# Kernel tuning notes

Measured on AMD Instinct MI355X. Metric: run time of the kernel, lower is better.

The kernel has to match this reference:

```python
import jax, jax.numpy as jnp
import numpy as np

B, T, I, H, O = 128, 256, 64, 512, 1
G = 4 * H


def setup_inputs() -> dict:
    key = jax.random.key(0)
    ks = jax.random.split(key, 16)
    s = 1.0 / np.sqrt(H)  # PyTorch LSTM/Linear init scale

    def u(k, shape):
        return jax.random.uniform(k, shape, jnp.float32, -s, s)

    return {
        "x": jax.random.normal(ks[0], (B, T, I), jnp.float32),
        "w_ih_0f": u(ks[1], (G, I)), "w_hh_0f": u(ks[2], (G, H)), "b_0f": u(ks[3], (G,)),
        "w_ih_0b": u(ks[4], (G, I)), "w_hh_0b": u(ks[5], (G, H)), "b_0b": u(ks[6], (G,)),
        "w_ih_1f": u(ks[7], (G, 2 * H)), "w_hh_1f": u(ks[8], (G, H)), "b_1f": u(ks[9], (G,)),
        "w_ih_1b": u(ks[10], (G, 2 * H)), "w_hh_1b": u(ks[11], (G, H)), "b_1b": u(ks[12], (G,)),
        "fc_w": u(ks[13], (O, 2 * H)), "fc_b": u(ks[14], (O,)),
    }


def _lstm_dir(x, w_ih, w_hh, b, reverse):
    # x: [B, T, F]. Precompute input projection for all timesteps (one big GEMM).
    xp = jnp.einsum('btf,gf->btg', x, w_ih) + b  # [B, T, 4H]

    def step(carry, xt):
        h, c = carry
        gates = xt + h @ w_hh.T  # [B, 4H]
        i, f, g, o = jnp.split(gates, 4, axis=-1)  # PyTorch gate order i,f,g,o
        c = jax.nn.sigmoid(f) * c + jax.nn.sigmoid(i) * jnp.tanh(g)
        h = jax.nn.sigmoid(o) * jnp.tanh(c)
        return (h, c), h

    h0 = jnp.zeros((x.shape[0], H), x.dtype)
    (_, _), hs = jax.lax.scan(step, (h0, h0), jnp.swapaxes(xp, 0, 1), reverse=reverse)
    return jnp.swapaxes(hs, 0, 1)  # [B, T, H], time-aligned with input


def reference(x, w_ih_0f, w_hh_0f, b_0f, w_ih_0b, w_hh_0b, b_0b,
              w_ih_1f, w_hh_1f, b_1f, w_ih_1b, w_hh_1b, b_1b, fc_w, fc_b):
    h = jnp.concatenate([_lstm_dir(x, w_ih_0f, w_hh_0f, b_0f, False),
                         _lstm_dir(x, w_ih_0b, w_hh_0b, b_0b, True)], axis=-1)
    h = jnp.concatenate([_lstm_dir(h, w_ih_1f, w_hh_1f, b_1f, False),
                         _lstm_dir(h, w_ih_1b, w_hh_1b, b_1b, True)], axis=-1)
    return h[:, -1, :] @ fc_w.T + fc_b  # [B, O]
```

## Files before the change

kernel.cpp:

```cpp
#include <hip/hip_runtime.h>

#define HB 65536
#define NBLK 256

typedef unsigned short u16;
typedef unsigned long long u64;
typedef __attribute__((ext_vector_type(8))) short bf16x8;
typedef __attribute__((ext_vector_type(8))) _Float16 f16x8;
typedef __attribute__((ext_vector_type(4))) float f32x4;
typedef __attribute__((ext_vector_type(2))) unsigned long long u64x2;
typedef __attribute__((ext_vector_type(8))) short s16x8;

#define MFMA_F16(a, b, c) __builtin_amdgcn_mfma_f32_16x16x32_f16(a, b, c, 0, 0, 0)
#define MFMA_BF16(a, b, c) __builtin_amdgcn_mfma_f32_16x16x32_bf16(a, b, c, 0, 0, 0)

__device__ __forceinline__ float fsig(float x) { return 1.f / (1.f + __expf(-x)); }
__device__ __forceinline__ float ftanh(float x) {
  float e = __expf(2.f * x);
  return 1.f - 2.f / (e + 1.f);
}
__device__ __forceinline__ u16 f2bf(float f) {
  unsigned u = __builtin_bit_cast(unsigned, f);
  return (u16)((u + 0x7FFFu + ((u >> 16) & 1)) >> 16);
}
__device__ __forceinline__ float bf2f(u16 h) {
  unsigned u = ((unsigned)h) << 16;
  return __builtin_bit_cast(float, u);
}
__device__ __forceinline__ u16 f2h(float f) {
  _Float16 h = (_Float16)f;
  return __builtin_bit_cast(u16, h);
}

__device__ __forceinline__ u64 at_ld64(const void* p) {
  return __hip_atomic_load((const u64*)p, __ATOMIC_RELAXED, __HIP_MEMORY_SCOPE_AGENT);
}
__device__ __forceinline__ void at_st64(void* p, u64 v) {
  __hip_atomic_store((u64*)p, v, __ATOMIC_RELAXED, __HIP_MEMORY_SCOPE_AGENT);
}
__device__ __forceinline__ unsigned at_ld32(const void* p) {
  return __hip_atomic_load((const unsigned*)p, __ATOMIC_RELAXED, __HIP_MEMORY_SCOPE_AGENT);
}
__device__ __forceinline__ void at_st32(void* p, unsigned v) {
  __hip_atomic_store((unsigned*)p, v, __ATOMIC_RELAXED, __HIP_MEMORY_SCOPE_AGENT);
}
__device__ __forceinline__ u64 pk4(u16 a, u16 b, u16 c, u16 d) {
  return (u64)a | ((u64)b << 16) | ((u64)c << 32) | ((u64)d << 48);
}
__device__ __forceinline__ u64 pkf2(float a, float b) {
  return (u64)__builtin_bit_cast(unsigned, a) | ((u64)__builtin_bit_cast(unsigned, b) << 32);
}

template <bool F16>
__global__ void pack_w(const float* __restrict__ W, u16* __restrict__ dst, int K) {
  int NKT = K >> 5;
  long gid = (long)blockIdx.x * 256 + threadIdx.x;
  long total = (long)128 * NKT * 64;
  if (gid >= total) return;
  int lane = gid & 63;
  int kt = (gid >> 6) % NKT;
  int rt = (gid >> 6) / NKT;
  int r = lane & 15;
  int grow = (r >> 2) * 512 + rt * 4 + (r & 3);
  int k0 = kt * 32 + (lane >> 4) * 8;
  long base = ((long)(rt * NKT + kt) * 2) * 512 + lane * 8;
#pragma unroll
  for (int e = 0; e < 8; ++e) {
    float w = W[(long)grow * K + k0 + e];
    u16 hi, lo;
    if (F16) {
      _Float16 h = (_Float16)w;
      hi = __builtin_bit_cast(u16, h);
      _Float16 l2 = (_Float16)(w - (float)h);
      lo = __builtin_bit_cast(u16, l2);
    } else {
      hi = f2bf(w);
      lo = f2bf(w - bf2f(hi));
    }
    dst[base + e] = hi;
    dst[base + 512 + e] = lo;
  }
}

__global__ void pack_x(const float* __restrict__ x, u16* __restrict__ xp) {
  long gid = (long)blockIdx.x * 256 + threadIdx.x;
  if (gid >= 128L * 256 * 64) return;
  int k = gid & 63;
  long bt = gid >> 6;
  int t = bt & 255;
  int b = bt >> 8;
  xp[((long)t * 128 + b) * 64 + k] = f2h(x[((long)b * 256 + t) * 64 + k]);
}

__global__ void pack_bias(const float* __restrict__ b0f, const float* __restrict__ b0b,
                          const float* __restrict__ b1f, const float* __restrict__ b1b,
                          float* __restrict__ bp) {
  int gid = blockIdx.x * 256 + threadIdx.x;
  if (gid >= 8192) return;
  int src = gid >> 11;
  int idx = gid & 2047;
  int rt = idx >> 4, rr = idx & 15;
  int grow = (rr >> 2) * 512 + rt * 4 + (rr & 3);
  const float* B = (src == 0) ? b0f : (src == 1) ? b0b : (src == 2) ? b1f : b1b;
  bp[gid] = B[grow];
}

#define C_TRANS 0
#define C_FIN 64

__global__ __launch_bounds__(512, 2) void lstm_persist(
    const u16* __restrict__ xpack, u16* __restrict__ h0arch,
    const u16* __restrict__ wih0f_p, const u16* __restrict__ wih0b_p,
    const u16* __restrict__ whh0f_p, const u16* __restrict__ whh0b_p,
    const u16* __restrict__ wih1f_p, const u16* __restrict__ whh1f_p,
    const u16* __restrict__ wih1b_p, const u16* __restrict__ whh1b_p,
    const float* __restrict__ biasP,
    u16* __restrict__ hl0, u16* __restrict__ hl1,
    float* __restrict__ h1bf32,
    const float* __restrict__ fcw, const float* __restrict__ fcb,
    float* __restrict__ out,
    unsigned* __restrict__ flagsA, unsigned* __restrict__ flagsB,
    unsigned* __restrict__ cnt) {
  const int bid = blockIdx.x;
  const int xcd = bid & 7, slot = bid >> 3;
  const int tid = threadIdx.x;
  const int wid = tid >> 6, l = tid & 63;
  const int c = l & 15, q = l >> 4;

  __shared__ __align__(16) char smem[65536];
  __shared__ __align__(16) f32x4 shacc[8][2][64];

  const f32x4 fz = {0.f, 0.f, 0.f, 0.f};

  auto arriveflag = [&](unsigned* fl, unsigned gen) {
    asm volatile("s_waitcnt vmcnt(0)" ::: "memory");
    __syncthreads();
    if (tid == 0) at_st32(fl + (long)bid * 64, gen);
  };
  auto waitflags = [&](const unsigned* fl, int base, int nmem, unsigned gen) {
    if (wid == 0) {
      unsigned f;
      do {
        f = (l < nmem) ? at_ld32(fl + (long)(base + l) * 64) : gen;
      } while (__ballot(f < gen));
    }
    __syncthreads();
  };
  auto arrivecnt = [&](int idx) {
    asm volatile("s_waitcnt vmcnt(0)" ::: "memory");
    __syncthreads();
    if (tid == 0)
      __hip_atomic_fetch_add(cnt + idx, 1u, __ATOMIC_RELAXED, __HIP_MEMORY_SCOPE_AGENT);
  };
  auto waitcnt_ = [&](int idx, unsigned tgt) {
    if (tid == 0) {
      while (at_ld32(cnt + idx) < tgt) __builtin_amdgcn_s_sleep(1);
    }
    __syncthreads();
  };

  {
    const int d = slot >> 4;
    const int bg = (slot >> 2) & 3;
    const int gbase = d * 128 + bg * 32;
    const int ug = xcd * 4 + (slot & 3);
    const int rowt = ug * 4 + (wid >> 1);
    const int kh = wid & 1;
    const u16* wxp = d ? wih0b_p : wih0f_p;
    const u16* whp = d ? whh0b_p : whh0f_p;
    const int b0e = bg * 32 + kh * 16;
    const float* bp = biasP + ((long)d * 128 + rowt) * 16 + q * 4;

    f16x8 wxh, wxl;
    {
      const u16* a = wxp + ((long)(rowt * 2 + kh) * 2) * 512 + l * 8;
      wxh = *(const f16x8*)a;
      wxl = *(const f16x8*)(a + 512);
    }
    bf16x8 whh_r[8], whl_r[8];
#pragma unroll
    for (int j = 0; j < 8; ++j) {
      const u16* a = whp + ((long)(rowt * 16 + kh * 8 + j) * 2) * 512 + l * 8;
      whh_r[j] = *(const bf16x8*)a;
      whl_r[j] = *(const bf16x8*)(a + 512);
    }

    const int sw = (c & 7) << 4;
    const int cq0 = (c << 10) | (q << 4);
    const int cq1 = ((16 + c) << 10) | (q << 4);

    float c_reg[4] = {0.f, 0.f, 0.f, 0.f};
    for (int s = 0; s < 256; ++s) {
      const int t = d ? 255 - s : s;
      const int par = s & 1;
      f32x4 acc0 = fz, acc1 = fz;
      {
        const u16* xb = xpack + ((long)t * 128 + bg * 32 + c) * 64 + kh * 32 + q * 8;
        f16x8 bx0 = *(const f16x8*)xb;
        f16x8 bx1 = *(const f16x8*)(xb + 16 * 64);
        acc0 = MFMA_F16(wxh, bx0, acc0);
        acc0 = MFMA_F16(wxl, bx0, acc0);
        acc1 = MFMA_F16(wxh, bx1, acc1);
        acc1 = MFMA_F16(wxl, bx1, acc1);
      }
      if (s) {
        waitflags(flagsA, gbase, 32, s);
        const u16* hp_hi = hl0 + ((long)(par * 2 + d) * 2) * HB;
        const u16* hp_lo = hp_hi + HB;
#pragma unroll
        for (int i = 0; i < 8; ++i) {
          int m = tid + (i << 9);
          int pl = m >> 11, r = m & 2047;
          int b = r >> 6, k16 = r & 63;
          const u16* src = (pl ? hp_lo : hp_hi) + (long)(bg * 32 + b) * 512 + k16 * 8;
          u64x2 v;
          v.x = at_ld64(src);
          v.y = at_ld64(src + 4);
          int dst = pl * 32768 + (((b << 10) | (k16 << 4)) ^ ((b & 7) << 4));
          *(u64x2*)(smem + dst) = v;
        }
        __syncthreads();
#pragma unroll
        for (int j = 0; j < 8; ++j) {
          const int kt = kh * 8 + j;
          const int b0a = (cq0 | (kt << 6)) ^ sw;
          const int b1a = (cq1 | (kt << 6)) ^ sw;
          bf16x8 bhi0 = *(const bf16x8*)(smem + b0a);
          bf16x8 blo0 = *(const bf16x8*)(smem + 32768 + b0a);
          bf16x8 bhi1 = *(const bf16x8*)(smem + b1a);
          bf16x8 blo1 = *(const bf16x8*)(smem + 32768 + b1a);
          acc0 = MFMA_BF16(whh_r[j], bhi0, acc0);
          acc0 = MFMA_BF16(whl_r[j], bhi0, acc0);
          acc0 = MFMA_BF16(whh_r[j], blo0, acc0);
          acc1 = MFMA_BF16(whh_r[j], bhi1, acc1);
          acc1 = MFMA_BF16(whl_r[j], bhi1, acc1);
          acc1 = MFMA_BF16(whh_r[j], blo1, acc1);
        }
      }
      shacc[wid][0][l] = acc0;
      shacc[wid][1][l] = acc1;
      __syncthreads();
      {
        const int pr = (wid >> 1) * 2;
        const int bo = wid & 1;
        f32x4 tot = shacc[pr][bo][l] + shacc[pr + 1][bo][l];
        float pre[4];
#pragma unroll
        for (int i = 0; i < 4; ++i) pre[i] = tot[i] + bp[i];
        const int par_w = par ^ 1;
        u16* hn_hi = hl0 + ((long)(par_w * 2 + d) * 2) * HB;
        u16* hn_lo = hn_hi + HB;
        const int b = b0e + c;
        u16 pbh[4], pbl[4], pf[4];
#pragma unroll
        for (int i = 0; i < 4; ++i) {
          float gI = __shfl(pre[i], c);
          float gF = __shfl(pre[i], c + 16);
          float gG = __shfl(pre[i], c + 32);
          float gO = __shfl(pre[i], c + 48);
          float cn = fsig(gF) * c_reg[i] + fsig(gI) * ftanh(gG);
          c_reg[i] = cn;
          float hv = fsig(gO) * ftanh(cn);
          u16 hh = f2bf(hv);
          pbh[i] = hh;
          pbl[i] = f2bf(hv - bf2f(hh));
          pf[i] = f2h(hv);
        }
        if (q == 0) {
          if (s < 255) {
            at_st64(hn_hi + (long)b * 512 + rowt * 4, pk4(pbh[0], pbh[1], pbh[2], pbh[3]));
            at_st64(hn_lo + (long)b * 512 + rowt * 4, pk4(pbl[0], pbl[1], pbl[2], pbl[3]));
          }
          at_st64(h0arch + ((long)t * 128 + b) * 1024 + d * 512 + rowt * 4,
                  pk4(pf[0], pf[1], pf[2], pf[3]));
        }
      }
      if (s < 255) arriveflag(flagsA, (unsigned)(s + 1));
      else arrivecnt(C_TRANS);
    }
  }
  waitcnt_(C_TRANS, NBLK);
  __threadfence();
  __syncthreads();

  {
    const int ug1 = xcd * 8 + (slot & 7);
    const int bg1 = slot >> 3;
    const int rl1 = (wid >> 1) & 1;
    const int btl1 = wid & 1;
    const int kh = wid >> 2;
    const int rowt1 = ug1 * 2 + rl1;
    const int b01 = bg1 * 32 + btl1 * 16;
    f32x4 a0 = fz, a1 = fz;
    const u16* bbase = h0arch + (255L * 128 + b01 + c) * 1024 + q * 8;
#pragma unroll
    for (int kk = 0; kk < 16; ++kk) {
      int kt = kh * 16 + kk;
      const u16* a = wih1b_p + ((long)(rowt1 * 32 + kt) * 2) * 512 + l * 8;
      f16x8 ahi = *(const f16x8*)a;
      f16x8 alo = *(const f16x8*)(a + 512);
      f16x8 bx = *(const f16x8*)(bbase + kt * 32);
      f32x4& t0 = (kk & 1) ? a1 : a0;
      t0 = MFMA_F16(ahi, bx, t0);
      t0 = MFMA_F16(alo, bx, t0);
    }
    f32x4 acc = a0 + a1;
    shacc[wid][0][l] = acc;
    __syncthreads();
    if (wid < 4) {
      f32x4 tot = shacc[wid][0][l] + shacc[wid + 4][0][l];
      const float* bp1 = biasP + (3L * 128 + rowt1) * 16 + q * 4;
      float pre[4];
#pragma unroll
      for (int i = 0; i < 4; ++i) pre[i] = tot[i] + bp1[i];
      const int b = b01 + c;
      float hv[4];
#pragma unroll
      for (int i = 0; i < 4; ++i) {
        float gI = __shfl(pre[i], c);
        float gG = __shfl(pre[i], c + 32);
        float gO = __shfl(pre[i], c + 48);
        float cn = fsig(gI) * ftanh(gG);
        hv[i] = fsig(gO) * ftanh(cn);
      }
      if (q == 0) {
        at_st64((u16*)(h1bf32 + (long)b * 512 + rowt1 * 4), pkf2(hv[0], hv[1]));
        at_st64((u16*)(h1bf32 + (long)b * 512 + rowt1 * 4 + 2), pkf2(hv[2], hv[3]));
      }
    }
    __syncthreads();
  }

  {
    const int ug1 = xcd * 8 + (slot & 7);
    const int bg1 = slot >> 3;
    const int g1base = bg1 * 64;
    const int rl1 = wid & 1;
    const int kh1 = wid >> 1;
    const int rowt1 = ug1 * 2 + rl1;

    f16x8 w1h[8], w1l[8];
#pragma unroll
    for (int j = 0; j < 8; ++j) {
      const u16* a = wih1f_p + ((long)(rowt1 * 32 + kh1 * 8 + j) * 2) * 512 + l * 8;
      w1h[j] = *(const f16x8*)a;
      w1l[j] = *(const f16x8*)(a + 512);
    }
    bf16x8 v1h[4], v1l[4];
#pragma unroll
    for (int j = 0; j < 4; ++j) {
      const u16* a = whh1f_p + ((long)(rowt1 * 16 + kh1 * 4 + j) * 2) * 512 + l * 8;
      v1h[j] = *(const bf16x8*)a;
      v1l[j] = *(const bf16x8*)(a + 512);
    }

    const int sw = (c & 7) << 4;
    const int cq0 = (c << 10) | (q << 4);
    const int cq1 = ((16 + c) << 10) | (q << 4);
    const int rl_o = wid & 1;
    const int bt_o = wid >> 1;
    const int rowt_o = ug1 * 2 + rl_o;
    const float* bp1 = biasP + (2L * 128 + rowt_o) * 16 + q * 4;

    float c_reg[4] = {0.f, 0.f, 0.f, 0.f};
    for (int s = 0; s < 256; ++s) {
      const int par = s & 1;
      f32x4 acc0 = fz, acc1 = fz;
      {
        const u16* hb = h0arch + ((long)s * 128 + bg1 * 32 + c) * 1024 + q * 8;
#pragma unroll
        for (int j = 0; j < 8; ++j) {
          const int kt = kh1 * 8 + j;
          f16x8 bx0 = *(const f16x8*)(hb + kt * 32);
          f16x8 bx1 = *(const f16x8*)(hb + 16 * 1024 + kt * 32);
          acc0 = MFMA_F16(w1h[j], bx0, acc0);
          acc0 = MFMA_F16(w1l[j], bx0, acc0);
          acc1 = MFMA_F16(w1h[j], bx1, acc1);
          acc1 = MFMA_F16(w1l[j], bx1, acc1);
        }
      }
      if (s) {
        waitflags(flagsB, g1base, 64, s);
        const u16* hp_hi = hl1 + (long)(par * 2) * HB;
        const u16* hp_lo = hp_hi + HB;
#pragma unroll
        for (int i = 0; i < 8; ++i) {
          int m = tid + (i << 9);
          int pl = m >> 11, r = m & 2047;
          int b = r >> 6, k16 = r & 63;
          const u16* src = (pl ? hp_lo : hp_hi) + (long)(bg1 * 32 + b) * 512 + k16 * 8;
          u64x2 v;
          v.x = at_ld64(src);
          v.y = at_ld64(src + 4);
          int dst = pl * 32768 + (((b << 10) | (k16 << 4)) ^ ((b & 7) << 4));
          *(u64x2*)(smem + dst) = v;
        }
        __syncthreads();
#pragma unroll
        for (int j = 0; j < 4; ++j) {
          const int kt = kh1 * 4 + j;
          const int b0a = (cq0 | (kt << 6)) ^ sw;
          const int b1a = (cq1 | (kt << 6)) ^ sw;
          bf16x8 bhi0 = *(const bf16x8*)(smem + b0a);
          bf16x8 blo0 = *(const bf16x8*)(smem + 32768 + b0a);
          bf16x8 bhi1 = *(const bf16x8*)(smem + b1a);
          bf16x8 blo1 = *(const bf16x8*)(smem + 32768 + b1a);
          acc0 = MFMA_BF16(v1h[j], bhi0, acc0);
          acc0 = MFMA_BF16(v1l[j], bhi0, acc0);
          acc0 = MFMA_BF16(v1h[j], blo0, acc0);
          acc1 = MFMA_BF16(v1h[j], bhi1, acc1);
          acc1 = MFMA_BF16(v1l[j], bhi1, acc1);
          acc1 = MFMA_BF16(v1h[j], blo1, acc1);
        }
      }
      shacc[wid][0][l] = acc0;
      shacc[wid][1][l] = acc1;
      __syncthreads();
      if (wid < 4) {
        f32x4 tot = shacc[rl_o][bt_o][l] + shacc[2 + rl_o][bt_o][l] +
                    shacc[4 + rl_o][bt_o][l] + shacc[6 + rl_o][bt_o][l];
        float pre[4];
#pragma unroll
        for (int i = 0; i < 4; ++i) pre[i] = tot[i] + bp1[i];
        const int par_w = par ^ 1;
        u16* hn_hi = hl1 + (long)(par_w * 2) * HB;
        u16* hn_lo = hn_hi + HB;
        const int b = bg1 * 32 + bt_o * 16 + c;
        u16 pbh[4], pbl[4];
#pragma unroll
        for (int i = 0; i < 4; ++i) {
          float gI = __shfl(pre[i], c);
          float gF = __shfl(pre[i], c + 16);
          float gG = __shfl(pre[i], c + 32);
          float gO = __shfl(pre[i], c + 48);
          float cn = fsig(gF) * c_reg[i] + fsig(gI) * ftanh(gG);
          c_reg[i] = cn;
          float hv = fsig(gO) * ftanh(cn);
          u16 hh = f2bf(hv);
          pbh[i] = hh;
          pbl[i] = f2bf(hv - bf2f(hh));
        }
        if (q == 0) {
          if (s < 255) {
            at_st64(hn_hi + (long)b * 512 + rowt_o * 4, pk4(pbh[0], pbh[1], pbh[2], pbh[3]));
            at_st64(hn_lo + (long)b * 512 + rowt_o * 4, pk4(pbl[0], pbl[1], pbl[2], pbl[3]));
          } else {
            at_st64(hl1 + (long)b * 512 + rowt_o * 4, pk4(pbh[0], pbh[1], pbh[2], pbh[3]));
            at_st64(hl1 + HB + (long)b * 512 + rowt_o * 4, pk4(pbl[0], pbl[1], pbl[2], pbl[3]));
          }
        }
      }
      if (s < 255) arriveflag(flagsB, (unsigned)(s + 1));
      else arrivecnt(C_FIN);
    }
  }
  waitcnt_(C_FIN, NBLK);

  if (bid < 128 && wid == 0) {
    const int b = bid;
    const int j0 = l * 8;
    u64x2 vh, vl;
    vh.x = at_ld64(hl1 + (long)b * 512 + j0);
    vh.y = at_ld64(hl1 + (long)b * 512 + j0 + 4);
    vl.x = at_ld64(hl1 + HB + (long)b * 512 + j0);
    vl.y = at_ld64(hl1 + HB + (long)b * 512 + j0 + 4);
    s16x8 hhi = __builtin_bit_cast(s16x8, vh);
    s16x8 hlo = __builtin_bit_cast(s16x8, vl);
    float ssum = 0.f;
#pragma unroll
    for (int e = 0; e < 8; ++e) {
      int j = j0 + e;
      float hf = bf2f((u16)hhi[e]) + bf2f((u16)hlo[e]);
      unsigned hbu = at_ld32(h1bf32 + (long)b * 512 + j);
      ssum += hf * fcw[j] + __builtin_bit_cast(float, hbu) * fcw[512 + j];
    }
#pragma unroll
    for (int off = 32; off; off >>= 1) ssum += __shfl_down(ssum, off);
    if (l == 0) out[b] = ssum + fcb[0];
  }
}

extern "C" void kernel_launch(void* const* d_in, const int* in_sizes, int n_in,
                              void* d_out, int out_size, void* d_ws, size_t ws_size,
                              hipStream_t stream) {
  const float* x     = (const float*)d_in[0];
  const float* wih0f = (const float*)d_in[1];
  const float* whh0f = (const float*)d_in[2];
  const float* b0f   = (const float*)d_in[3];
  const float* wih0b = (const float*)d_in[4];
  const float* whh0b = (const float*)d_in[5];
  const float* b0b   = (const float*)d_in[6];
  const float* wih1f = (const float*)d_in[7];
  const float* whh1f = (const float*)d_in[8];
  const float* b1f   = (const float*)d_in[9];
  const float* wih1b = (const float*)d_in[10];
  const float* whh1b = (const float*)d_in[11];
  const float* b1b   = (const float*)d_in[12];
  const float* fcw   = (const float*)d_in[13];
  const float* fcb   = (const float*)d_in[14];
  float* out = (float*)d_out;

  char* p = (char*)d_ws;
  auto alloc = [&](size_t bytes) {
    char* r = p;
    p += (bytes + 255) & ~(size_t)255;
    return r;
  };
  u16* xpack   = (u16*)alloc(128L * 256 * 64 * 2);
  u16* wih0f_p = (u16*)alloc(128L * 2 * 2 * 512 * 2);
  u16* wih0b_p = (u16*)alloc(128L * 2 * 2 * 512 * 2);
  u16* whh0f_p = (u16*)alloc(128L * 16 * 2 * 512 * 2);
  u16* whh0b_p = (u16*)alloc(128L * 16 * 2 * 512 * 2);
  u16* wih1f_p = (u16*)alloc(128L * 32 * 2 * 512 * 2);
  u16* whh1f_p = (u16*)alloc(128L * 16 * 2 * 512 * 2);
  u16* wih1b_p = (u16*)alloc(128L * 32 * 2 * 512 * 2);
  u16* whh1b_p = (u16*)alloc(128L * 16 * 2 * 512 * 2);
  float* biasP = (float*)alloc(8192 * 4);
  u16* hl0     = (u16*)alloc(2L * 2 * 2 * HB * 2);
  u16* hl1     = (u16*)alloc(2L * 2 * HB * 2);
  float* h1bf32= (float*)alloc((long)HB * 4);
  unsigned* flagsA = (unsigned*)alloc(256L * 64 * 4);
  unsigned* flagsB = (unsigned*)alloc(256L * 64 * 4);
  unsigned* cnt    = (unsigned*)alloc(128 * 4);
  u16* h0arch  = (u16*)alloc(256L * 128 * 1024 * 2);

  pack_w<true><<<64, 256, 0, stream>>>(wih0f, wih0f_p, 64);
  pack_w<true><<<64, 256, 0, stream>>>(wih0b, wih0b_p, 64);
  pack_w<false><<<512, 256, 0, stream>>>(whh0f, whh0f_p, 512);
  pack_w<false><<<512, 256, 0, stream>>>(whh0b, whh0b_p, 512);
  pack_w<true><<<1024, 256, 0, stream>>>(wih1f, wih1f_p, 1024);
  pack_w<true><<<1024, 256, 0, stream>>>(wih1b, wih1b_p, 1024);
  pack_w<false><<<512, 256, 0, stream>>>(whh1f, whh1f_p, 512);
  pack_w<false><<<512, 256, 0, stream>>>(whh1b, whh1b_p, 512);
  pack_x<<<8192, 256, 0, stream>>>(x, xpack);
  pack_bias<<<32, 256, 0, stream>>>(b0f, b0b, b1f, b1b, biasP);

  (void)hipMemsetAsync(flagsA, 0, 256L * 64 * 4, stream);
  (void)hipMemsetAsync(flagsB, 0, 256L * 64 * 4, stream);
  (void)hipMemsetAsync(cnt, 0, 128 * 4, stream);

  lstm_persist<<<NBLK, 512, 0, stream>>>(
      xpack, h0arch,
      wih0f_p, wih0b_p, whh0f_p, whh0b_p,
      wih1f_p, whh1f_p, wih1b_p, whh1b_p,
      biasP, hl0, hl1, h1bf32,
      fcw, fcb, out, flagsA, flagsB, cnt);
}
```

Before: 3.817 ms.

## Interleave hi/lo bf16 hidden planes and use 128-bit coherent loads/stores

Hidden-state hi and lo bf16 halves are interleaved into one plane with 8-element chunks (4 hi, 4 lo), so each producer writes one 16-byte store instead of two 8-byte atomics. Consumers stage the plane into LDS with batched global_load_dwordx4 using sc0 sc1 cache bits, waiting on all loads at once, and split hi/lo into separate LDS regions. This is meant to cut per-step latency on the cross-block hidden-state exchange in the recurrent loop. It relies on inline asm cache-coherence bits instead of atomics for visibility across blocks.

```diff
diff --git a/kernel.cpp b/kernel.cpp
--- a/kernel.cpp
+++ b/kernel.cpp
@@ -1,7 +1,7 @@
 #include <hip/hip_runtime.h>
 
-#define HB 65536
 #define NBLK 256
+#define PLANE 131072
 
 typedef unsigned short u16;
 typedef unsigned long long u64;
@@ -9,7 +9,6 @@
 typedef __attribute__((ext_vector_type(8))) _Float16 f16x8;
 typedef __attribute__((ext_vector_type(4))) float f32x4;
 typedef __attribute__((ext_vector_type(2))) unsigned long long u64x2;
-typedef __attribute__((ext_vector_type(8))) short s16x8;
 
 #define MFMA_F16(a, b, c) __builtin_amdgcn_mfma_f32_16x16x32_f16(a, b, c, 0, 0, 0)
 #define MFMA_BF16(a, b, c) __builtin_amdgcn_mfma_f32_16x16x32_bf16(a, b, c, 0, 0, 0)
@@ -49,6 +48,9 @@
 }
 __device__ __forceinline__ u64 pkf2(float a, float b) {
   return (u64)__builtin_bit_cast(unsigned, a) | ((u64)__builtin_bit_cast(unsigned, b) << 32);
+}
+__device__ __forceinline__ void st128_cp(u16* p, u64x2 v) {
+  asm volatile("global_store_dwordx4 %0, %1, off sc0 sc1" :: "v"(p), "v"(v) : "memory");
 }
 
 template <bool F16>
@@ -158,6 +160,27 @@
     }
     __syncthreads();
   };
+  auto stage16 = [&](const u16* plane, int b0blk) {
+    u64x2 vv[8];
+#pragma unroll
+    for (int i = 0; i < 8; ++i) {
+      int m = tid + (i << 9);
+      int b = m >> 7, cb = m & 127;
+      const u16* src = plane + ((long)(b0blk + b) << 10) + (cb << 3);
+      asm volatile("global_load_dwordx4 %0, %1, off sc0 sc1"
+                   : "=v"(vv[i]) : "v"(src) : "memory");
+    }
+    asm volatile("s_waitcnt vmcnt(0)" ::: "memory");
+    __builtin_amdgcn_sched_barrier(0);
+#pragma unroll
+    for (int i = 0; i < 8; ++i) {
+      int m = tid + (i << 9);
+      int b = m >> 7, cb = m & 127;
+      int ahi = ((b << 10) | (cb << 3)) ^ ((b & 7) << 4);
+      *(u64*)(smem + ahi) = vv[i].x;
+      *(u64*)(smem + 32768 + ahi) = vv[i].y;
+    }
+  };
 
   {
     const int d = slot >> 4;
@@ -205,20 +228,7 @@
       }
       if (s) {
         waitflags(flagsA, gbase, 32, s);
-        const u16* hp_hi = hl0 + ((long)(par * 2 + d) * 2) * HB;
-        const u16* hp_lo = hp_hi + HB;
-#pragma unroll
-        for (int i = 0; i < 8; ++i) {
-          int m = tid + (i << 9);
-          int pl = m >> 11, r = m & 2047;
-          int b = r >> 6, k16 = r & 63;
-          const u16* src = (pl ? hp_lo : hp_hi) + (long)(bg * 32 + b) * 512 + k16 * 8;
-          u64x2 v;
-          v.x = at_ld64(src);
-          v.y = at_ld64(src + 4);
-          int dst = pl * 32768 + (((b << 10) | (k16 << 4)) ^ ((b & 7) << 4));
-          *(u64x2*)(smem + dst) = v;
-        }
+        stage16(hl0 + (long)(par * 2 + d) * PLANE, bg * 32);
         __syncthreads();
 #pragma unroll
         for (int j = 0; j < 8; ++j) {
@@ -248,8 +258,7 @@
 #pragma unroll
         for (int i = 0; i < 4; ++i) pre[i] = tot[i] + bp[i];
         const int par_w = par ^ 1;
-        u16* hn_hi = hl0 + ((long)(par_w * 2 + d) * 2) * HB;
-        u16* hn_lo = hn_hi + HB;
+        u16* hn = hl0 + (long)(par_w * 2 + d) * PLANE;
         const int b = b0e + c;
         u16 pbh[4], pbl[4], pf[4];
 #pragma unroll
@@ -268,8 +277,10 @@
         }
         if (q == 0) {
           if (s < 255) {
-            at_st64(hn_hi + (long)b * 512 + rowt * 4, pk4(pbh[0], pbh[1], pbh[2], pbh[3]));
-            at_st64(hn_lo + (long)b * 512 + rowt * 4, pk4(pbl[0], pbl[1], pbl[2], pbl[3]));
+            u64x2 pv;
+            pv.x = pk4(pbh[0], pbh[1], pbh[2], pbh[3]);
+            pv.y = pk4(pbl[0], pbl[1], pbl[2], pbl[3]);
+            st128_cp(hn + ((long)b << 10) + rowt * 8, pv);
           }
           at_st64(h0arch + ((long)t * 128 + b) * 1024 + d * 512 + rowt * 4,
                   pk4(pf[0], pf[1], pf[2], pf[3]));
@@ -381,20 +392,7 @@
       }
       if (s) {
         waitflags(flagsB, g1base, 64, s);
-        const u16* hp_hi = hl1 + (long)(par * 2) * HB;
-        const u16* hp_lo = hp_hi + HB;
-#pragma unroll
-        for (int i = 0; i < 8; ++i) {
-          int m = tid + (i << 9);
-          int pl = m >> 11, r = m & 2047;
-          int b = r >> 6, k16 = r & 63;
-          const u16* src = (pl ? hp_lo : hp_hi) + (long)(bg1 * 32 + b) * 512 + k16 * 8;
-          u64x2 v;
-          v.x = at_ld64(src);
-          v.y = at_ld64(src + 4);
-          int dst = pl * 32768 + (((b << 10) | (k16 << 4)) ^ ((b & 7) << 4));
-          *(u64x2*)(smem + dst) = v;
-        }
+        stage16(hl1 + (long)par * PLANE, bg1 * 32);
         __syncthreads();
 #pragma unroll
         for (int j = 0; j < 4; ++j) {
@@ -423,8 +421,7 @@
 #pragma unroll
         for (int i = 0; i < 4; ++i) pre[i] = tot[i] + bp1[i];
         const int par_w = par ^ 1;
-        u16* hn_hi = hl1 + (long)(par_w * 2) * HB;
-        u16* hn_lo = hn_hi + HB;
+        u16* hn = hl1 + (long)par_w * PLANE;
         const int b = bg1 * 32 + bt_o * 16 + c;
         u16 pbh[4], pbl[4];
 #pragma unroll
@@ -441,13 +438,10 @@
           pbl[i] = f2bf(hv - bf2f(hh));
         }
         if (q == 0) {
-          if (s < 255) {
-            at_st64(hn_hi + (long)b * 512 + rowt_o * 4, pk4(pbh[0], pbh[1], pbh[2], pbh[3]));
-            at_st64(hn_lo + (long)b * 512 + rowt_o * 4, pk4(pbl[0], pbl[1], pbl[2], pbl[3]));
-          } else {
-            at_st64(hl1 + (long)b * 512 + rowt_o * 4, pk4(pbh[0], pbh[1], pbh[2], pbh[3]));
-            at_st64(hl1 + HB + (long)b * 512 + rowt_o * 4, pk4(pbl[0], pbl[1], pbl[2], pbl[3]));
-          }
+          u64x2 pv;
+          pv.x = pk4(pbh[0], pbh[1], pbh[2], pbh[3]);
+          pv.y = pk4(pbl[0], pbl[1], pbl[2], pbl[3]);
+          st128_cp(hn + ((long)b << 10) + rowt_o * 8, pv);
         }
       }
       if (s < 255) arriveflag(flagsB, (unsigned)(s + 1));
@@ -458,19 +452,19 @@
 
   if (bid < 128 && wid == 0) {
     const int b = bid;
-    const int j0 = l * 8;
-    u64x2 vh, vl;
-    vh.x = at_ld64(hl1 + (long)b * 512 + j0);
-    vh.y = at_ld64(hl1 + (long)b * 512 + j0 + 4);
-    vl.x = at_ld64(hl1 + HB + (long)b * 512 + j0);
-    vl.y = at_ld64(hl1 + HB + (long)b * 512 + j0 + 4);
-    s16x8 hhi = __builtin_bit_cast(s16x8, vh);
-    s16x8 hlo = __builtin_bit_cast(s16x8, vl);
+    const int c0 = l * 2;
+    const u16* pl0 = hl1 + ((long)b << 10);
+    u64 h0 = at_ld64(pl0 + c0 * 8);
+    u64 l0_ = at_ld64(pl0 + c0 * 8 + 4);
+    u64 h1 = at_ld64(pl0 + (c0 + 1) * 8);
+    u64 l1_ = at_ld64(pl0 + (c0 + 1) * 8 + 4);
     float ssum = 0.f;
 #pragma unroll
     for (int e = 0; e < 8; ++e) {
-      int j = j0 + e;
-      float hf = bf2f((u16)hhi[e]) + bf2f((u16)hlo[e]);
+      int j = l * 8 + e;
+      u16 hh = (u16)(((e < 4 ? h0 : h1) >> ((e & 3) * 16)) & 0xFFFF);
+      u16 hl_ = (u16)(((e < 4 ? l0_ : l1_) >> ((e & 3) * 16)) & 0xFFFF);
+      float hf = bf2f(hh) + bf2f(hl_);
       unsigned hbu = at_ld32(h1bf32 + (long)b * 512 + j);
       ssum += hf * fcw[j] + __builtin_bit_cast(float, hbu) * fcw[512 + j];
     }
@@ -516,9 +510,9 @@
   u16* wih1b_p = (u16*)alloc(128L * 32 * 2 * 512 * 2);
   u16* whh1b_p = (u16*)alloc(128L * 16 * 2 * 512 * 2);
   float* biasP = (float*)alloc(8192 * 4);
-  u16* hl0     = (u16*)alloc(2L * 2 * 2 * HB * 2);
-  u16* hl1     = (u16*)alloc(2L * 2 * HB * 2);
-  float* h1bf32= (float*)alloc((long)HB * 4);
+  u16* hl0     = (u16*)alloc(4L * PLANE * 2);
+  u16* hl1     = (u16*)alloc(2L * PLANE * 2);
+  float* h1bf32= (float*)alloc(128L * 512 * 4);
   unsigned* flagsA = (unsigned*)alloc(256L * 64 * 4);
   unsigned* flagsB = (unsigned*)alloc(256L * 64 * 4);
   unsigned* cnt    = (unsigned*)alloc(128 * 4);
```

Result: faster. 3.125 ms (-18.1%).
